# Kernel tuning notes

Hardware: AMD Instinct MI355X
Metric: run time of the kernel (lower is better)

## Reference

```python
import jax, jax.numpy as jnp
from jax import lax
import numpy as np

B, C, H, W = 1, 128, 32, 32
OC, K = 128, 3
STRIDE, PAD, DIL = 1, 1, 1
ARRAY_SIZE = 32
QUANT = 8


def setup_inputs() -> dict:
    key = jax.random.key(0)
    k1, k2, k3 = jax.random.split(key, 3)
    x = jax.random.normal(k1, (B, C, H, W), dtype=jnp.float32)
    weight = jax.random.normal(k2, (OC, C, K, K), dtype=jnp.float32) * 0.05
    bias = jax.random.normal(k3, (OC,), dtype=jnp.float32) * 0.05
    return {"x": x, "weight": weight, "bias": bias}


def _conv(x, w, b):
    out = lax.conv_general_dilated(
        x, w, window_strides=(STRIDE, STRIDE),
        padding=((PAD, PAD), (PAD, PAD)),
        rhs_dilation=(DIL, DIL),
        dimension_numbers=("NCHW", "OIHW", "NCHW"))
    return out + b[None, :, None, None]


def _unfold(x, oh, ow):
    # torch F.unfold: (B, C*K*K, L) with channel-major ordering (c, kh, kw)
    xp = jnp.pad(x, ((0, 0), (0, 0), (PAD, PAD), (PAD, PAD)))
    cols = jnp.stack(
        [xp[:, :, i:i + oh, j:j + ow] for i in range(K) for j in range(K)],
        axis=2)  # (B, C, K*K, OH, OW)
    return cols.reshape(B, C * K * K, oh * ow)


def reference(x, weight, bias):
    oh = (H + 2 * PAD - DIL * (K - 1) - 1) // STRIDE + 1
    ow = (W + 2 * PAD - DIL * (K - 1) - 1) // STRIDE + 1
    L = oh * ow
    qmax = float(2 ** QUANT - 1)

    # --- set_quant_params: per-spatial-location scale/zero_point from full conv out ---
    out_full = _conv(x, weight, bias).reshape(1, OC, -1)  # (1, OC, L)
    mx = jnp.max(out_full, axis=1)  # (1, L)
    mn = jnp.min(out_full, axis=1)
    scale = (mx - mn) / qmax
    zp = jnp.clip(-mn / scale, 0.0, qmax)
    zp = jnp.where(jnp.isnan(zp), 0.0, zp)
    zp = jnp.trunc(zp)  # .int() truncation
    scale = lax.stop_gradient(scale)[:, None, None, :]  # (1,1,1,L)
    zp = lax.stop_gradient(zp)[:, None, None, :]

    # --- unfold + explicit elementwise multiply (crossbar expansion) ---
    cols = _unfold(x, oh, ow)                       # (B, C*K*K, L)
    pre = cols[:, None, :, :] * weight.reshape(1, OC, C * K * K, 1)  # (B,OC,CKK,L)

    # pad front of dim 2 to a multiple of array_size (pads a full chunk if divisible)
    ckk = C * K * K
    pad_d3 = ARRAY_SIZE - ckk % ARRAY_SIZE
    pre = jnp.pad(pre, ((0, 0), (0, 0), (pad_d3, 0), (0, 0)))

    # block-sum over array_size chunks (crossbar partial sums)
    n_chunks = (ckk + pad_d3) // ARRAY_SIZE
    accu = pre.reshape(B, OC, n_chunks, ARRAY_SIZE, L).sum(axis=3)  # (B,OC,n_chunks,L)

    # per-chunk fake-quant (Quant8F) with straight-through estimator
    q = jnp.clip(jnp.round(accu / scale) + zp, 0.0, qmax)
    deq = (q - zp) * scale
    quant_accu = accu + lax.stop_gradient(deq - accu)

    # reduce over chunks -> conv output (note: bias is NOT added in original forward)
    return quant_accu.sum(axis=2).reshape(B, OC, oh, ow)
```

## Files before the change

kernel.cpp:

```cpp
#include <hip/hip_runtime.h>

#define L_     1024
#define CKK_   1152
#define QMAX_  255.0f
#define NCH    36
#define PSTR_  (131072 + 64)

__global__ __launch_bounds__(256) void gemm_chunks(
    const float* __restrict__ x,
    const float* __restrict__ w,
    float* __restrict__ planes)
{
    __shared__ __align__(16) float Wb[32][132];
    __shared__ __align__(16) float xs[32][64];

    const int t   = threadIdx.x;
    const int l0  = blockIdx.x * 64;
    const int j   = blockIdx.y;
    const int d0  = j * 32;
    const int oh0 = l0 >> 5;

    float4 wld[4];
    int    wo[4], wk[4];
#pragma unroll
    for (int it = 0; it < 4; it++) {
        const int f4 = it * 256 + t;
        wo[it]  = f4 >> 3;
        wk[it]  = (f4 & 7) * 4;
        wld[it] = *(const float4*)(w + wo[it] * CKK_ + d0 + wk[it]);
    }

    float xl[8];
    int   xk[8], xll[8];
#pragma unroll
    for (int it = 0; it < 8; it++) {
        const int e  = it * 256 + t;
        const int k  = e >> 6, ll = e & 63;
        const int d  = d0 + k;
        const int c  = d / 9, r = d - 9 * c;
        const int kh = r / 3, kw = r - 3 * kh;
        const int iy = oh0 + (ll >> 5) + kh - 1;
        const int ix = (ll & 31) + kw - 1;
        const bool ok = ((unsigned)iy < 32u) & ((unsigned)ix < 32u);
        const int idx = ok ? (c * 1024 + iy * 32 + ix) : 0;
        const float v = x[idx];
        xl[it] = ok ? v : 0.f;
        xk[it] = k; xll[it] = ll;
    }

#pragma unroll
    for (int it = 0; it < 4; it++) {
        Wb[wk[it] + 0][wo[it]] = wld[it].x;
        Wb[wk[it] + 1][wo[it]] = wld[it].y;
        Wb[wk[it] + 2][wo[it]] = wld[it].z;
        Wb[wk[it] + 3][wo[it]] = wld[it].w;
    }
#pragma unroll
    for (int it = 0; it < 8; it++)
        xs[xk[it]][xll[it]] = xl[it];
    __syncthreads();

    const int oc0 = (t & 31) * 4;
    const int ll0 = (t >> 5) * 8;
    float acc[4][8];
#pragma unroll
    for (int r = 0; r < 4; r++)
#pragma unroll
        for (int i = 0; i < 8; i++) acc[r][i] = 0.f;

#pragma unroll
    for (int k = 0; k < 32; k++) {
        const float4 wv = *(const float4*)&Wb[k][oc0];
        const float4 xa = *(const float4*)&xs[k][ll0];
        const float4 xb = *(const float4*)&xs[k][ll0 + 4];
        acc[0][0] = fmaf(wv.x, xa.x, acc[0][0]);
        acc[0][1] = fmaf(wv.x, xa.y, acc[0][1]);
        acc[0][2] = fmaf(wv.x, xa.z, acc[0][2]);
        acc[0][3] = fmaf(wv.x, xa.w, acc[0][3]);
        acc[0][4] = fmaf(wv.x, xb.x, acc[0][4]);
        acc[0][5] = fmaf(wv.x, xb.y, acc[0][5]);
        acc[0][6] = fmaf(wv.x, xb.z, acc[0][6]);
        acc[0][7] = fmaf(wv.x, xb.w, acc[0][7]);
        acc[1][0] = fmaf(wv.y, xa.x, acc[1][0]);
        acc[1][1] = fmaf(wv.y, xa.y, acc[1][1]);
        acc[1][2] = fmaf(wv.y, xa.z, acc[1][2]);
        acc[1][3] = fmaf(wv.y, xa.w, acc[1][3]);
        acc[1][4] = fmaf(wv.y, xb.x, acc[1][4]);
        acc[1][5] = fmaf(wv.y, xb.y, acc[1][5]);
        acc[1][6] = fmaf(wv.y, xb.z, acc[1][6]);
        acc[1][7] = fmaf(wv.y, xb.w, acc[1][7]);
        acc[2][0] = fmaf(wv.z, xa.x, acc[2][0]);
        acc[2][1] = fmaf(wv.z, xa.y, acc[2][1]);
        acc[2][2] = fmaf(wv.z, xa.z, acc[2][2]);
        acc[2][3] = fmaf(wv.z, xa.w, acc[2][3]);
        acc[2][4] = fmaf(wv.z, xb.x, acc[2][4]);
        acc[2][5] = fmaf(wv.z, xb.y, acc[2][5]);
        acc[2][6] = fmaf(wv.z, xb.z, acc[2][6]);
        acc[2][7] = fmaf(wv.z, xb.w, acc[2][7]);
        acc[3][0] = fmaf(wv.w, xa.x, acc[3][0]);
        acc[3][1] = fmaf(wv.w, xa.y, acc[3][1]);
        acc[3][2] = fmaf(wv.w, xa.z, acc[3][2]);
        acc[3][3] = fmaf(wv.w, xa.w, acc[3][3]);
        acc[3][4] = fmaf(wv.w, xb.x, acc[3][4]);
        acc[3][5] = fmaf(wv.w, xb.y, acc[3][5]);
        acc[3][6] = fmaf(wv.w, xb.z, acc[3][6]);
        acc[3][7] = fmaf(wv.w, xb.w, acc[3][7]);
    }

    float* dst = planes + (size_t)j * PSTR_ + (size_t)l0 * 128;
#pragma unroll
    for (int i = 0; i < 8; i++)
        *(float4*)(dst + (ll0 + i) * 128 + oc0) =
            make_float4(acc[0][i], acc[1][i], acc[2][i], acc[3][i]);
}

__global__ __launch_bounds__(256) void fused_mq(
    const float* __restrict__ planes,
    const float* __restrict__ bias,
    float* __restrict__ out)
{
    __shared__ float part[256];
    __shared__ float mnb[128], mxb[128];
    __shared__ float s_sc, s_zp, s_iv;
    const int t  = threadIdx.x;
    const int oc = t & 127, jh = t >> 7;
    const int l  = blockIdx.x;

    const float* p = planes + (size_t)(jh * 18) * PSTR_ + (size_t)l * 128 + oc;
    float v[18];
#pragma unroll
    for (int j = 0; j < 18; j++) v[j] = p[(size_t)j * PSTR_];

    float s = 0.f;
#pragma unroll
    for (int j = 0; j < 18; j++) s += v[j];
    part[t] = s;
    __syncthreads();

    if (t < 128) {
        const float tot = part[t] + part[t + 128] + bias[t];
        mnb[t] = tot;
        mxb[t] = tot;
    }
    __syncthreads();
#pragma unroll
    for (int st = 64; st > 0; st >>= 1) {
        if (t < st) {
            mnb[t] = fminf(mnb[t], mnb[t + st]);
            mxb[t] = fmaxf(mxb[t], mxb[t + st]);
        }
        __syncthreads();
    }
    if (t == 0) {
        const float amn = mnb[0], amx = mxb[0];
        const float sv  = (amx - amn) / QMAX_;
        float z = -amn / sv;
        z = fmaxf(z, 0.f);
        z = fminf(z, QMAX_);
        z = truncf(z);
        s_sc = sv;
        s_zp = z;
        s_iv = 1.0f / sv;
    }
    __syncthreads();

    const float sc = s_sc, zv = s_zp, iv = s_iv;
    float q = 0.f;
#pragma unroll
    for (int j = 0; j < 18; j++) {
        float qn = rintf(v[j] * iv) + zv;
        qn = fminf(fmaxf(qn, 0.f), QMAX_);
        q += (qn - zv) * sc;
    }
    part[t] = q;
    __syncthreads();

    if (t < 128)
        out[oc * L_ + l] = part[t] + part[t + 128];
}

template <bool QUANT>
__global__ __launch_bounds__(256) void cas_direct(
    const float* __restrict__ x, const float* __restrict__ w,
    float* __restrict__ out, const float* __restrict__ scale,
    const float* __restrict__ zp, const float* __restrict__ inv)
{
    const int t = threadIdx.x;
    const int ocBase = blockIdx.x * 16;
    const int l = blockIdx.y * 256 + t;
    const int oh = l >> 5, ow = l & 31;

    float sc = 0.f, zv = 0.f, iv = 0.f;
    if (QUANT) { sc = scale[l]; zv = zp[l]; iv = inv[l]; }

    float acc[16];
#pragma unroll
    for (int oc = 0; oc < 16; oc++) acc[oc] = 0.f;

    for (int j = 0; j < NCH; j++) {
        const int d0 = j * 32;
        float xv[32];
#pragma unroll
        for (int dd = 0; dd < 32; dd++) {
            const int d = d0 + dd, c = d / 9, r = d - 9 * c;
            const int kh = r / 3, kw = r - 3 * kh;
            const int off = c * 1024 + (kh - 1) * 32 + (kw - 1);
            const bool ok = ((unsigned)(oh + kh - 1) < 32u) &
                            ((unsigned)(ow + kw - 1) < 32u);
            const int idx = ok ? (off + l) : 0;
            const float vv = x[idx];
            xv[dd] = ok ? vv : 0.f;
        }
#pragma unroll
        for (int oc = 0; oc < 16; oc++) {
            const float4* wp = (const float4*)(w + (ocBase + oc) * CKK_ + d0);
            float pa = 0.f, pb = 0.f;
#pragma unroll
            for (int k4 = 0; k4 < 8; k4++) {
                const float4 wv = wp[k4];
                float& pr = (k4 < 4) ? pa : pb;
                pr = fmaf(wv.x, xv[4 * k4 + 0], pr);
                pr = fmaf(wv.y, xv[4 * k4 + 1], pr);
                pr = fmaf(wv.z, xv[4 * k4 + 2], pr);
                pr = fmaf(wv.w, xv[4 * k4 + 3], pr);
            }
            const float s2 = pa + pb;
            if (QUANT) {
                float qn = rintf(s2 * iv) + zv;
                qn = fminf(fmaxf(qn, 0.f), QMAX_);
                acc[oc] += (qn - zv) * sc;
            } else {
                acc[oc] += s2;
            }
        }
    }
#pragma unroll
    for (int oc = 0; oc < 16; oc++)
        out[(ocBase + oc) * L_ + l] = acc[oc];
}

__global__ __launch_bounds__(256) void minmax_conv(
    const float* __restrict__ conv, const float* __restrict__ bias,
    float* __restrict__ scale, float* __restrict__ zp, float* __restrict__ inv)
{
    __shared__ float smn[16][17], smx[16][17];
    const int t = threadIdx.x, li = t & 15, g = t >> 4;
    const int l = blockIdx.x * 16 + li;
    float mn = INFINITY, mx = -INFINITY;
#pragma unroll
    for (int i = 0; i < 8; i++) {
        const int oc = g * 8 + i;
        const float v = conv[oc * L_ + l] + bias[oc];
        mn = fminf(mn, v); mx = fmaxf(mx, v);
    }
    smn[g][li] = mn; smx[g][li] = mx;
    __syncthreads();
    if (t < 16) {
        const int l2 = blockIdx.x * 16 + t;
        float amn = smn[0][t], amx = smx[0][t];
#pragma unroll
        for (int g2 = 1; g2 < 16; g2++) {
            amn = fminf(amn, smn[g2][t]); amx = fmaxf(amx, smx[g2][t]);
        }
        const float s = (amx - amn) / QMAX_;
        float z = -amn / s;
        z = fminf(fmaxf(z, 0.f), QMAX_);
        z = truncf(z);
        scale[l2] = s; zp[l2] = z; inv[l2] = 1.0f / s;
    }
}

extern "C" void kernel_launch(void* const* d_in, const int* in_sizes, int n_in,
                              void* d_out, int out_size, void* d_ws, size_t ws_size,
                              hipStream_t stream) {
    const float* x    = (const float*)d_in[0];
    const float* w    = (const float*)d_in[1];
    const float* bias = (const float*)d_in[2];
    float* out = (float*)d_out;
    float* ws  = (float*)d_ws;

    const size_t main_need = (size_t)NCH * PSTR_ * 4;
    if (ws_size >= main_need) {
        float* planes = ws;
        gemm_chunks<<<dim3(16, NCH), 256, 0, stream>>>(x, w, planes);
        fused_mq<<<1024, 256, 0, stream>>>(planes, bias, out);
    } else {
        float* conv  = ws;
        float* scale = conv + 131072;
        float* zpv   = scale + 1024;
        float* inv   = zpv + 1024;
        cas_direct<false><<<dim3(8, 4), 256, 0, stream>>>(x, w, conv, nullptr, nullptr, nullptr);
        minmax_conv<<<64, 256, 0, stream>>>(conv, bias, scale, zpv, inv);
        cas_direct<true><<<dim3(8, 4), 256, 0, stream>>>(x, w, out, scale, zpv, inv);
    }
}
```

Measured before the change: 74.86 us.

## Store chunk partial sums location-major and process two pixels per reduction block

Partial-sum planes are now laid out with each spatial location's 36 chunks and 128 channels contiguous, replacing separate per-chunk planes. The quantization kernel handles two output locations per block, with each thread reading all 36 chunks for one channel. Min/max uses wavefront shuffles instead of a shared-memory tree, and output is written as float2 with a block index swizzle. This reduces synchronisation and improves store coalescing, at the cost of more registers per thread and a larger write stride in the GEMM epilogue.

```diff
diff --git a/kernel.cpp b/kernel.cpp
--- a/kernel.cpp
+++ b/kernel.cpp
@@ -4,7 +4,7 @@
 #define CKK_   1152
 #define QMAX_  255.0f
 #define NCH    36
-#define PSTR_  (131072 + 64)
+#define LSTR_  (NCH * 128)
 
 __global__ __launch_bounds__(256) void gemm_chunks(
     const float* __restrict__ x,
@@ -107,10 +107,10 @@
         acc[3][7] = fmaf(wv.w, xb.w, acc[3][7]);
     }
 
-    float* dst = planes + (size_t)j * PSTR_ + (size_t)l0 * 128;
+    float* dst = planes + (size_t)(l0 + ll0) * LSTR_ + (size_t)j * 128 + oc0;
 #pragma unroll
     for (int i = 0; i < 8; i++)
-        *(float4*)(dst + (ll0 + i) * 128 + oc0) =
+        *(float4*)(dst + (size_t)i * LSTR_) =
             make_float4(acc[0][i], acc[1][i], acc[2][i], acc[3][i]);
 }
 
@@ -119,64 +119,62 @@
     const float* __restrict__ bias,
     float* __restrict__ out)
 {
-    __shared__ float part[256];
-    __shared__ float mnb[128], mxb[128];
-    __shared__ float s_sc, s_zp, s_iv;
+    __shared__ float red[8];
+    __shared__ float sp[2][3];
+    __shared__ float qb[2][128];
     const int t  = threadIdx.x;
-    const int oc = t & 127, jh = t >> 7;
-    const int l  = blockIdx.x;
-
-    const float* p = planes + (size_t)(jh * 18) * PSTR_ + (size_t)l * 128 + oc;
-    float v[18];
-#pragma unroll
-    for (int j = 0; j < 18; j++) v[j] = p[(size_t)j * PSTR_];
+    const int b  = blockIdx.x;
+    const int m  = (b & 15) * 32 + (b >> 4);
+    const int l0 = m << 1;
+    const int oc = t & 127, px = t >> 7;
+    const int l  = l0 + px;
+
+    const float* p = planes + (size_t)l * LSTR_ + oc;
+    float v[36];
+#pragma unroll
+    for (int j = 0; j < 36; j++) v[j] = p[(size_t)j * 128];
 
     float s = 0.f;
 #pragma unroll
-    for (int j = 0; j < 18; j++) s += v[j];
-    part[t] = s;
-    __syncthreads();
-
-    if (t < 128) {
-        const float tot = part[t] + part[t + 128] + bias[t];
-        mnb[t] = tot;
-        mxb[t] = tot;
-    }
-    __syncthreads();
-#pragma unroll
-    for (int st = 64; st > 0; st >>= 1) {
-        if (t < st) {
-            mnb[t] = fminf(mnb[t], mnb[t + st]);
-            mxb[t] = fmaxf(mxb[t], mxb[t + st]);
-        }
-        __syncthreads();
-    }
-    if (t == 0) {
-        const float amn = mnb[0], amx = mxb[0];
+    for (int j = 0; j < 36; j++) s += v[j];
+    const float tot = s + bias[oc];
+
+    float mn = tot, mx = tot;
+#pragma unroll
+    for (int off = 32; off > 0; off >>= 1) {
+        mn = fminf(mn, __shfl_xor(mn, off));
+        mx = fmaxf(mx, __shfl_xor(mx, off));
+    }
+    const int wv = t >> 6;
+    if ((t & 63) == 0) { red[wv] = mn; red[4 + wv] = mx; }
+    __syncthreads();
+
+    if ((t & 127) == 0) {
+        const int w0 = px << 1;
+        const float amn = fminf(red[w0], red[w0 + 1]);
+        const float amx = fmaxf(red[4 + w0], red[4 + w0 + 1]);
         const float sv  = (amx - amn) / QMAX_;
         float z = -amn / sv;
         z = fmaxf(z, 0.f);
         z = fminf(z, QMAX_);
         z = truncf(z);
-        s_sc = sv;
-        s_zp = z;
-        s_iv = 1.0f / sv;
-    }
-    __syncthreads();
-
-    const float sc = s_sc, zv = s_zp, iv = s_iv;
+        sp[px][0] = sv; sp[px][1] = z; sp[px][2] = 1.0f / sv;
+    }
+    __syncthreads();
+
+    const float sc = sp[px][0], zv = sp[px][1], iv = sp[px][2];
     float q = 0.f;
 #pragma unroll
-    for (int j = 0; j < 18; j++) {
+    for (int j = 0; j < 36; j++) {
         float qn = rintf(v[j] * iv) + zv;
         qn = fminf(fmaxf(qn, 0.f), QMAX_);
         q += (qn - zv) * sc;
     }
-    part[t] = q;
+    qb[px][oc] = q;
     __syncthreads();
 
     if (t < 128)
-        out[oc * L_ + l] = part[t] + part[t + 128];
+        *(float2*)(out + (size_t)t * L_ + l0) = make_float2(qb[0][t], qb[1][t]);
 }
 
 template <bool QUANT>
@@ -279,11 +277,11 @@
     float* out = (float*)d_out;
     float* ws  = (float*)d_ws;
 
-    const size_t main_need = (size_t)NCH * PSTR_ * 4;
+    const size_t main_need = (size_t)L_ * LSTR_ * 4;
     if (ws_size >= main_need) {
         float* planes = ws;
         gemm_chunks<<<dim3(16, NCH), 256, 0, stream>>>(x, w, planes);
-        fused_mq<<<1024, 256, 0, stream>>>(planes, bias, out);
+        fused_mq<<<512, 256, 0, stream>>>(planes, bias, out);
     } else {
         float* conv  = ws;
         float* scale = conv + 131072;
```

New measurement: 76.33 us. About the same (+2.0%).
